# Kernel tuning notes

Measured on AMD Instinct MI355X. Metric: run time of the kernel, lower is better.

Reference implementation:

```python
import jax, jax.numpy as jnp
import numpy as np


def setup_inputs() -> dict:
    key = jax.random.key(0)
    k1, k2, k3 = jax.random.split(key, 3)
    N, B, DEG, F = 100000, 10000, 32, 256
    nodes = jax.random.randint(k1, (B,), 0, N, dtype=jnp.int32)
    neighbor_idx = jax.random.randint(k2, (B, DEG), 0, N, dtype=jnp.int32)
    features = jax.random.normal(k3, (N, F), dtype=jnp.float32)
    return {"nodes": nodes, "neighbor_idx": neighbor_idx, "features": features}


def reference(nodes, neighbor_idx, features):
    # union of {neighbors} and {self}, deduplicated (dense mask set-to-1 is idempotent)
    idx = jnp.concatenate([neighbor_idx, nodes[:, None]], axis=1)  # [B, D+1]
    sidx = jnp.sort(idx, axis=1)
    first = jnp.concatenate(
        [jnp.ones((sidx.shape[0], 1), bool), sidx[:, 1:] != sidx[:, :-1]], axis=1
    )  # True at first occurrence of each unique index
    feats = features[sidx]  # [B, D+1, F] gather
    w = first.astype(features.dtype)
    num = jnp.einsum("bd,bdf->bf", w, feats)
    den = w.sum(axis=1, keepdims=True)
    return num / den
```

## Files before the change

kernel.cpp:

```cpp
#include <hip/hip_runtime.h>

#define DEG 32
#define NIDX 33
#define F 256

__global__ __launch_bounds__(256) void aggregator_kernel(
    const int* __restrict__ nodes,
    const int* __restrict__ nbr,
    const float* __restrict__ feats,
    float* __restrict__ out,
    int B)
{
    const int b    = blockIdx.x;
    const int tid  = threadIdx.x;
    const int wid  = tid >> 6;
    const int lane = tid & 63;

    __shared__ int   s_idx[NIDX];
    __shared__ float s_w[NIDX];
    __shared__ float s_feat[NIDX][F];

    if (tid < NIDX)
        s_idx[tid] = (tid < DEG) ? nbr[(size_t)b * DEG + tid] : nodes[b];
    __syncthreads();

    for (int d = wid; d < NIDX; d += 4) {
        const float* g = feats + (size_t)s_idx[d] * F + lane * 4;
        __builtin_amdgcn_global_load_lds(
            (const __attribute__((address_space(1))) void*)g,
            (__attribute__((address_space(3))) void*)&s_feat[d][0],
            16 , 0, 0);
    }

    if (tid < NIDX) {
        const int v = s_idx[tid];
        float w = 1.0f;
        for (int j = 0; j < tid; ++j)
            if (s_idx[j] == v) { w = 0.0f; break; }
        s_w[tid] = w;
    }
    __syncthreads();

    float acc = 0.0f, den = 0.0f;
    #pragma unroll
    for (int d = 0; d < NIDX; ++d) {
        const float w = s_w[d];
        den += w;
        acc = fmaf(w, s_feat[d][tid], acc);
    }
    out[(size_t)b * F + tid] = acc / den;
}

extern "C" void kernel_launch(void* const* d_in, const int* in_sizes, int n_in,
                              void* d_out, int out_size, void* d_ws, size_t ws_size,
                              hipStream_t stream)
{
    const int*   nodes = (const int*)d_in[0];
    const int*   nbr   = (const int*)d_in[1];
    const float* feats = (const float*)d_in[2];
    float*       out   = (float*)d_out;

    const int B = in_sizes[0];

    aggregator_kernel<<<B, 256, 0, stream>>>(nodes, nbr, feats, out, B);
}
```

Before: 52.44 us.

## Split feature columns across two blocks per row and compute weights via ballot

Each output row is now handled by two blocks, one per 128-column half, so the grid doubles and each block holds about half the shared memory. That lets more blocks fit per CU and gives more gathers in flight. The dedup weights become a wavefront ballot mask with popcount for the denominator, which drops the shared weight array. The accumulation splits the 33 neighbours between the two 128-thread halves and combines them through shared memory. The costs are re-reading the index row twice per row, an extra barrier, and half-row (512-byte) gather segments.

After: 59.54 us. 13.5% more time.

```diff
diff --git a/kernel.cpp b/kernel.cpp
--- a/kernel.cpp
+++ b/kernel.cpp
@@ -1,8 +1,9 @@
 #include <hip/hip_runtime.h>
 
-#define DEG 32
-#define NIDX 33
-#define F 256
+#define DEG   32
+#define NIDX  33
+#define F     256
+#define HCOLS 128
 
 __global__ __launch_bounds__(256) void aggregator_kernel(
     const int* __restrict__ nodes,
@@ -11,44 +12,56 @@
     float* __restrict__ out,
     int B)
 {
-    const int b    = blockIdx.x;
     const int tid  = threadIdx.x;
-    const int wid  = tid >> 6;
+    const int w    = tid >> 6;
     const int lane = tid & 63;
+    const int r    = blockIdx.x >> 1;
+    const int h    = blockIdx.x & 1;
 
-    __shared__ int   s_idx[NIDX];
-    __shared__ float s_w[NIDX];
-    __shared__ float s_feat[NIDX][F];
+    __shared__ int s_idx[NIDX + 1];
+    __shared__ __align__(16) float s_half[NIDX + 1][HCOLS];
+    __shared__ float s_part[HCOLS];
 
     if (tid < NIDX)
-        s_idx[tid] = (tid < DEG) ? nbr[(size_t)b * DEG + tid] : nodes[b];
+        s_idx[tid] = (tid < DEG) ? nbr[(size_t)r * DEG + tid] : nodes[r];
     __syncthreads();
 
-    for (int d = wid; d < NIDX; d += 4) {
-        const float* g = feats + (size_t)s_idx[d] * F + lane * 4;
+    for (int p = w; p <= 16; p += 4) {
+        const int d  = 2 * p;
+        const int dl = d + (lane >> 5);
+        const int di = (dl <= 32) ? dl : 32;
+        const float* g = feats + (size_t)s_idx[di] * F + h * HCOLS + (lane & 31) * 4;
         __builtin_amdgcn_global_load_lds(
             (const __attribute__((address_space(1))) void*)g,
-            (__attribute__((address_space(3))) void*)&s_feat[d][0],
-            16 , 0, 0);
+            (__attribute__((address_space(3))) void*)&s_half[d][0],
+            16, 0, 0);
     }
 
-    if (tid < NIDX) {
-        const int v = s_idx[tid];
-        float w = 1.0f;
-        for (int j = 0; j < tid; ++j)
-            if (s_idx[j] == v) { w = 0.0f; break; }
-        s_w[tid] = w;
+    int first = 0;
+    if (lane < NIDX) {
+        const int v = s_idx[lane];
+        first = 1;
+        for (int j = 0; j < lane; ++j)
+            if (s_idx[j] == v) { first = 0; break; }
     }
+    const unsigned long long mask = __ballot(first);
+    const float den = (float)__popcll(mask);
+
     __syncthreads();
 
-    float acc = 0.0f, den = 0.0f;
-    #pragma unroll
-    for (int d = 0; d < NIDX; ++d) {
-        const float w = s_w[d];
-        den += w;
-        acc = fmaf(w, s_feat[d][tid], acc);
+    const int c  = tid & (HCOLS - 1);
+    const int g0 = (tid >> 7) * 17;
+    const int ng = 17 - (tid >> 7);
+    float acc = 0.0f;
+    for (int j = 0; j < ng; ++j) {
+        const int d = g0 + j;
+        const float wv = ((mask >> d) & 1ull) ? 1.0f : 0.0f;
+        acc = fmaf(wv, s_half[d][c], acc);
     }
-    out[(size_t)b * F + tid] = acc / den;
+    if (tid >= HCOLS) s_part[c] = acc;
+    __syncthreads();
+    if (tid < HCOLS)
+        out[(size_t)r * F + h * HCOLS + c] = (acc + s_part[c]) / den;
 }
 
 extern "C" void kernel_launch(void* const* d_in, const int* in_sizes, int n_in,
@@ -62,5 +75,5 @@
 
     const int B = in_sizes[0];
 
-    aggregator_kernel<<<B, 256, 0, stream>>>(nodes, nbr, feats, out, B);
+    aggregator_kernel<<<2 * B, 256, 0, stream>>>(nodes, nbr, feats, out, B);
 }
```
